# Kernel optimization log

Hardware: AMD Instinct MI355X
Metric: run time of the kernel (lower is better)

Reference implementation:

```python
import jax
import jax.numpy as jnp
from jax import lax
import numpy as np

HEADS = 12
GROUPS = 3
KSIZE = 5  # depthwise kernel for offset prediction


def bilinear_sample(img, grid):
    """img: (G,C,H,W); grid: (G,Hk,Wk,2) with (x,y) coords in [-1,1], align_corners=True.
    Returns (G,C,Hk*Wk). Coords are pre-clipped to [-1,1], so clamped indexing is exact."""
    G, C, H, W = img.shape
    gx = (grid[..., 0] + 1.0) * 0.5 * (W - 1)
    gy = (grid[..., 1] + 1.0) * 0.5 * (H - 1)
    x0 = jnp.floor(gx); y0 = jnp.floor(gy)
    wx1 = gx - x0; wx0 = 1.0 - wx1
    wy1 = gy - y0; wy0 = 1.0 - wy1
    x0i = jnp.clip(x0, 0, W - 1).astype(jnp.int32)
    x1i = jnp.clip(x0 + 1, 0, W - 1).astype(jnp.int32)
    y0i = jnp.clip(y0, 0, H - 1).astype(jnp.int32)
    y1i = jnp.clip(y0 + 1, 0, H - 1).astype(jnp.int32)
    flat = img.reshape(G, C, H * W)
    def gather(yi, xi):
        idx = (yi * W + xi).reshape(G, 1, -1)  # (G,1,Hk*Wk)
        return jnp.take_along_axis(flat, jnp.broadcast_to(idx, (G, C, idx.shape[-1])), axis=2)
    n = gx.shape[1] * gx.shape[2]
    w00 = (wy0 * wx0).reshape(G, 1, n); w01 = (wy0 * wx1).reshape(G, 1, n)
    w10 = (wy1 * wx0).reshape(G, 1, n); w11 = (wy1 * wx1).reshape(G, 1, n)
    return (gather(y0i, x0i) * w00 + gather(y0i, x1i) * w01 +
            gather(y1i, x0i) * w10 + gather(y1i, x1i) * w11)


def setup_inputs() -> dict:
    key = jax.random.key(0)
    ks = jax.random.split(key, 16)
    B, C, H, W = 8, 384, 32, 32
    Cg = C // GROUPS
    s = 0.02
    inp = {
        "x1": jax.random.normal(ks[0], (B, C, H, W), jnp.float32),
        "x2": jax.random.normal(ks[1], (B, C, H, W), jnp.float32),
        "wq": jax.random.normal(ks[2], (C, C), jnp.float32) * s,
        "bq": jnp.zeros((C,), jnp.float32),
        "w_off_dw": jax.random.normal(ks[3], (Cg, 1, KSIZE, KSIZE), jnp.float32) * s,
        "b_off_dw": jnp.zeros((Cg,), jnp.float32),
        "w_off_pw": jax.random.normal(ks[4], (2, Cg), jnp.float32) * s,
        "b_off_pw": jnp.zeros((2,), jnp.float32),
        "wk": jax.random.normal(ks[5], (C, C), jnp.float32) * s,
        "bk": jnp.zeros((C,), jnp.float32),
        "wv": jax.random.normal(ks[6], (C, C), jnp.float32) * s,
        "bv": jnp.zeros((C,), jnp.float32),
        "wo": jax.random.normal(ks[7], (C, C), jnp.float32) * s,
        "bo": jnp.zeros((C,), jnp.float32),
    }
    return inp


def deformable_cross_attn(x1, x2, wq, bq, w_off_dw, b_off_dw, w_off_pw, b_off_pw,
                          wk, bk, wv, bv, wo, bo):
    B, C, H, W = x1.shape
    Cg = C // GROUPS
    hc = C // HEADS
    scale = hc ** -0.5
    N = H * W
    # query projection (1x1 conv)
    q = jnp.einsum('oc,bchw->bohw', wq, x1) + bq[None, :, None, None]
    # grouped offset prediction: depthwise conv -> GELU -> 1x1 conv to 2 channels
    qg = q.reshape(B * GROUPS, Cg, H, W)
    off = lax.conv_general_dilated(qg, w_off_dw, (1, 1), 'SAME',
                                   feature_group_count=Cg,
                                   dimension_numbers=('NCHW', 'OIHW', 'NCHW'))
    off = jax.nn.gelu(off + b_off_dw[None, :, None, None])
    off = jnp.einsum('oc,bchw->bohw', w_off_pw, off) + b_off_pw[None, :, None, None]  # (B*G,2,H,W)
    dx = jnp.tanh(off[:, 0]) * (2.0 / W)
    dy = jnp.tanh(off[:, 1]) * (2.0 / H)
    ref_x = (jnp.arange(W, dtype=jnp.float32) + 0.5) / W * 2.0 - 1.0
    ref_y = (jnp.arange(H, dtype=jnp.float32) + 0.5) / H * 2.0 - 1.0
    px = jnp.clip(ref_x[None, None, :] + dx, -1.0, 1.0)
    py = jnp.clip(ref_y[None, :, None] + dy, -1.0, 1.0)
    grid = jnp.stack([px, py], axis=-1)  # (B*G,H,W,2)
    # sample key/value source at deformed positions
    x2g = x2.reshape(B * GROUPS, Cg, H, W)
    sampled = bilinear_sample(x2g, grid).reshape(B, C, N)
    k = jnp.einsum('oc,bcn->bon', wk, sampled) + bk[None, :, None]
    v = jnp.einsum('oc,bcn->bon', wv, sampled) + bv[None, :, None]
    qf = q.reshape(B, HEADS, hc, N)
    kf = k.reshape(B, HEADS, hc, N)
    vf = v.reshape(B, HEADS, hc, N)
    attn = jax.nn.softmax(jnp.einsum('bhcn,bhcm->bhnm', qf, kf) * scale, axis=-1)
    out = jnp.einsum('bhnm,bhcm->bhcn', attn, vf).reshape(B, C, H, W)
    y = jnp.einsum('oc,bchw->bohw', wo, out) + bo[None, :, None, None]
    return x1 + y, attn


def reference(x1, x2, wq, bq, w_off_dw, b_off_dw, w_off_pw, b_off_pw,
              wk, bk, wv, bv, wo, bo):
    return deformable_cross_attn(x1, x2, wq, bq, w_off_dw, b_off_dw,
                                 w_off_pw, b_off_pw, wk, bk, wv, bv, wo, bo)
```

## Files before the change

kernel.cpp:

```cpp
#include <hip/hip_runtime.h>
#include <hip/hip_bf16.h>

static constexpr int B = 8;
static constexpr int C = 384;
static constexpr int H = 32;
static constexpr int W = 32;
static constexpr int N = 1024;
static constexpr int Cg = 128;
static constexpr int HEADS = 12;
static constexpr int BG = 24;
static constexpr float SCALE = 0.17677669529663687f;

typedef short bf16x8 __attribute__((ext_vector_type(8)));
typedef float f32x4 __attribute__((ext_vector_type(4)));

__device__ __forceinline__ unsigned short bf16_bits(float x) {
    __hip_bfloat16 h = __float2bfloat16(x);
    return __builtin_bit_cast(unsigned short, h);
}
__device__ __forceinline__ float bf2f(unsigned short u) {
    return __builtin_bit_cast(float, ((unsigned)u) << 16);
}
__device__ __forceinline__ float fast_tanh(float x) {
    float e = __expf(2.0f * x);
    return 1.0f - 2.0f / (e + 1.0f);
}

__global__ __launch_bounds__(256) void prep(const float* __restrict__ wq,
                                            const float* __restrict__ wk,
                                            const float* __restrict__ wv,
                                            const float* __restrict__ wo,
                                            const float* __restrict__ x1,
                                            unsigned short* __restrict__ w16,
                                            unsigned short* __restrict__ x1T)
{
    __shared__ float tile[32][132];
    const int bx = blockIdx.x;
    const int tid = threadIdx.x;
    if (bx < 288) {
        int which = bx / 72, blk = bx - which*72;
        const float* src = (which == 0) ? wq : (which == 1) ? wk : (which == 2) ? wv : wo;
        int idx = (blk*256 + tid) * 8;
        const float4* p = (const float4*)(src + idx);
        float4 f0 = p[0], f1 = p[1];
        uint4 u;
        u.x = (unsigned)bf16_bits(f0.x) | ((unsigned)bf16_bits(f0.y) << 16);
        u.y = (unsigned)bf16_bits(f0.z) | ((unsigned)bf16_bits(f0.w) << 16);
        u.z = (unsigned)bf16_bits(f1.x) | ((unsigned)bf16_bits(f1.y) << 16);
        u.w = (unsigned)bf16_bits(f1.z) | ((unsigned)bf16_bits(f1.w) << 16);
        *(uint4*)(w16 + (size_t)which * 147456 + idx) = u;
        return;
    }
    const int xi = bx - 288;
    const int n0 = (xi & 7) * 128;
    const int t = xi >> 3;
    const int c0 = (t % 12) * 32;
    const int b = t / 12;
    {
        int c = tid >> 3, nq = (tid & 7) * 16;
        const float* sp = x1 + ((size_t)b*C + c0 + c)*N + n0 + nq;
        #pragma unroll
        for (int i = 0; i < 4; ++i)
            *(float4*)&tile[c][nq + 4*i] = *(const float4*)(sp + 4*i);
    }
    __syncthreads();
    {
        int n = tid >> 1, cb = (tid & 1) * 16;
        unsigned short* dp = x1T + ((size_t)b*N + n0 + n)*C + c0 + cb;
        #pragma unroll
        for (int half = 0; half < 2; ++half) {
            bf16x8 v;
            #pragma unroll
            for (int j = 0; j < 8; ++j)
                v[j] = (short)bf16_bits(tile[cb + half*8 + j][n]);
            *(bf16x8*)(dp + half*8) = v;
        }
    }
}

template<int MODE>
__global__ __launch_bounds__(256) void proj_mfma(const unsigned short* __restrict__ XT,
                                                 const unsigned short* __restrict__ Wb,
                                                 const float* __restrict__ bias,
                                                 const float* __restrict__ res,
                                                 void* __restrict__ out,
                                                 void* __restrict__ out2)
{
    __shared__ __align__(16) char smem[64*72*2*2];
    unsigned short* sA = (unsigned short*)smem;
    unsigned short* sB = sA + 64*72;
    float* ep = (float*)smem;

    const int tid = threadIdx.x;
    const int lane = tid & 63, w = tid >> 6;
    const int l15 = lane & 15, lq = lane >> 4;
    const int n0 = blockIdx.x * 64, o0 = blockIdx.y * 64, b = blockIdx.z;
    const int qn = (w & 1) * 32, qo = (w >> 1) * 32;

    const unsigned short* xg = XT + ((size_t)b*N + n0)*C;
    const unsigned short* wg = Wb + (size_t)o0*C;

    const f32x4 zero = {0.f, 0.f, 0.f, 0.f};
    f32x4 a00 = zero, a01 = zero, a10 = zero, a11 = zero;

    const int r = tid >> 2, c8 = (tid & 3) * 8;
    for (int c0 = 0; c0 < C; c0 += 64) {
        __syncthreads();
        *(bf16x8*)(sA + r*72 + c8)      = *(const bf16x8*)(xg + (size_t)r*C + c0 + c8);
        *(bf16x8*)(sA + r*72 + c8 + 32) = *(const bf16x8*)(xg + (size_t)r*C + c0 + c8 + 32);
        *(bf16x8*)(sB + r*72 + c8)      = *(const bf16x8*)(wg + (size_t)r*C + c0 + c8);
        *(bf16x8*)(sB + r*72 + c8 + 32) = *(const bf16x8*)(wg + (size_t)r*C + c0 + c8 + 32);
        __syncthreads();
        #pragma unroll
        for (int ks = 0; ks < 2; ++ks) {
            bf16x8 fa0 = *(const bf16x8*)(sA + (qn + l15)*72      + ks*32 + lq*8);
            bf16x8 fa1 = *(const bf16x8*)(sA + (qn + 16 + l15)*72 + ks*32 + lq*8);
            bf16x8 fb0 = *(const bf16x8*)(sB + (qo + l15)*72      + ks*32 + lq*8);
            bf16x8 fb1 = *(const bf16x8*)(sB + (qo + 16 + l15)*72 + ks*32 + lq*8);
            a00 = __builtin_amdgcn_mfma_f32_16x16x32_bf16(fa0, fb0, a00, 0, 0, 0);
            a01 = __builtin_amdgcn_mfma_f32_16x16x32_bf16(fa0, fb1, a01, 0, 0, 0);
            a10 = __builtin_amdgcn_mfma_f32_16x16x32_bf16(fa1, fb0, a10, 0, 0, 0);
            a11 = __builtin_amdgcn_mfma_f32_16x16x32_bf16(fa1, fb1, a11, 0, 0, 0);
        }
    }
    __syncthreads();
    #pragma unroll
    for (int rr = 0; rr < 4; ++rr) {
        int nr0 = qn + 4*lq + rr, nr1 = qn + 16 + 4*lq + rr;
        ep[nr0*65 + qo + l15]      = a00[rr];
        ep[nr0*65 + qo + 16 + l15] = a01[rr];
        ep[nr1*65 + qo + l15]      = a10[rr];
        ep[nr1*65 + qo + 16 + l15] = a11[rr];
    }
    __syncthreads();

    if constexpr (MODE == 3) {
        {
            int n = tid >> 2, ch = tid & 3;
            unsigned short* op = (unsigned short*)out + ((size_t)b*N + n0 + n)*C + o0;
            #pragma unroll
            for (int half = 0; half < 2; ++half) {
                int ob = ch*8 + half*32;
                bf16x8 v;
                #pragma unroll
                for (int j = 0; j < 8; ++j)
                    v[j] = (short)bf16_bits(ep[n*65 + ob + j] + bias[o0 + ob + j]);
                *(bf16x8*)(op + ob) = v;
            }
        }
        {
            int o = tid >> 2, nc = (tid & 3) * 16;
            float bz = bias[o0 + o];
            unsigned short* dp = (unsigned short*)out2 + ((size_t)b*C + o0 + o)*N + n0 + nc;
            #pragma unroll
            for (int half = 0; half < 2; ++half) {
                bf16x8 v;
                #pragma unroll
                for (int j = 0; j < 8; ++j)
                    v[j] = (short)bf16_bits(ep[(nc + half*8 + j)*65 + o] + bz);
                *(bf16x8*)(dp + half*8) = v;
            }
        }
    } else {
        int o = tid >> 2, nc = (tid & 3) * 16;
        float bz = bias[o0 + o];
        size_t base = ((size_t)b*C + o0 + o)*N + n0 + nc;
        #pragma unroll
        for (int i = 0; i < 4; ++i) {
            float4 rv = *(const float4*)(res + base + 4*i);
            f32x4 v;
            v[0] = ep[(nc + 4*i + 0)*65 + o] + bz + rv.x;
            v[1] = ep[(nc + 4*i + 1)*65 + o] + bz + rv.y;
            v[2] = ep[(nc + 4*i + 2)*65 + o] + bz + rv.z;
            v[3] = ep[(nc + 4*i + 3)*65 + o] + bz + rv.w;
            __builtin_nontemporal_store(v, (f32x4*)((float*)out + base + 4*i));
        }
    }
}

__global__ __launch_bounds__(256) void proj_kv(const unsigned short* __restrict__ XT,
                                               const unsigned short* __restrict__ Wk,
                                               const float* __restrict__ bk,
                                               const unsigned short* __restrict__ Wv,
                                               const float* __restrict__ bv,
                                               unsigned short* __restrict__ K16,
                                               unsigned short* __restrict__ V16)
{
    __shared__ __align__(16) char smem[64*72*2*3];
    unsigned short* sA  = (unsigned short*)smem;
    unsigned short* sBk = sA + 64*72;
    unsigned short* sBv = sA + 2*64*72;
    float* ep = (float*)smem;

    const int tid = threadIdx.x;
    const int lane = tid & 63, w = tid >> 6;
    const int l15 = lane & 15, lq = lane >> 4;
    const int n0 = blockIdx.x * 64, o0 = blockIdx.y * 64, b = blockIdx.z;
    const int qn = (w & 1) * 32, qo = (w >> 1) * 32;

    const unsigned short* xg = XT + ((size_t)b*N + n0)*C;
    const unsigned short* wkg = Wk + (size_t)o0*C;
    const unsigned short* wvg = Wv + (size_t)o0*C;

    const f32x4 zero = {0.f, 0.f, 0.f, 0.f};
    f32x4 k00 = zero, k01 = zero, k10 = zero, k11 = zero;
    f32x4 v00 = zero, v01 = zero, v10 = zero, v11 = zero;

    const int r = tid >> 2, c8 = (tid & 3) * 8;
    for (int c0 = 0; c0 < C; c0 += 64) {
        __syncthreads();
        *(bf16x8*)(sA  + r*72 + c8)      = *(const bf16x8*)(xg  + (size_t)r*C + c0 + c8);
        *(bf16x8*)(sA  + r*72 + c8 + 32) = *(const bf16x8*)(xg  + (size_t)r*C + c0 + c8 + 32);
        *(bf16x8*)(sBk + r*72 + c8)      = *(const bf16x8*)(wkg + (size_t)r*C + c0 + c8);
        *(bf16x8*)(sBk + r*72 + c8 + 32) = *(const bf16x8*)(wkg + (size_t)r*C + c0 + c8 + 32);
        *(bf16x8*)(sBv + r*72 + c8)      = *(const bf16x8*)(wvg + (size_t)r*C + c0 + c8);
        *(bf16x8*)(sBv + r*72 + c8 + 32) = *(const bf16x8*)(wvg + (size_t)r*C + c0 + c8 + 32);
        __syncthreads();
        #pragma unroll
        for (int ks = 0; ks < 2; ++ks) {
            bf16x8 fa0 = *(const bf16x8*)(sA + (qn + l15)*72      + ks*32 + lq*8);
            bf16x8 fa1 = *(const bf16x8*)(sA + (qn + 16 + l15)*72 + ks*32 + lq*8);
            bf16x8 fk0 = *(const bf16x8*)(sBk + (qo + l15)*72      + ks*32 + lq*8);
            bf16x8 fk1 = *(const bf16x8*)(sBk + (qo + 16 + l15)*72 + ks*32 + lq*8);
            bf16x8 fv0 = *(const bf16x8*)(sBv + (qo + l15)*72      + ks*32 + lq*8);
            bf16x8 fv1 = *(const bf16x8*)(sBv + (qo + 16 + l15)*72 + ks*32 + lq*8);
            k00 = __builtin_amdgcn_mfma_f32_16x16x32_bf16(fa0, fk0, k00, 0, 0, 0);
            k01 = __builtin_amdgcn_mfma_f32_16x16x32_bf16(fa0, fk1, k01, 0, 0, 0);
            k10 = __builtin_amdgcn_mfma_f32_16x16x32_bf16(fa1, fk0, k10, 0, 0, 0);
            k11 = __builtin_amdgcn_mfma_f32_16x16x32_bf16(fa1, fk1, k11, 0, 0, 0);
            v00 = __builtin_amdgcn_mfma_f32_16x16x32_bf16(fa0, fv0, v00, 0, 0, 0);
            v01 = __builtin_amdgcn_mfma_f32_16x16x32_bf16(fa0, fv1, v01, 0, 0, 0);
            v10 = __builtin_amdgcn_mfma_f32_16x16x32_bf16(fa1, fv0, v10, 0, 0, 0);
            v11 = __builtin_amdgcn_mfma_f32_16x16x32_bf16(fa1, fv1, v11, 0, 0, 0);
        }
    }
    __syncthreads();
    #pragma unroll
    for (int rr = 0; rr < 4; ++rr) {
        int nr0 = qn + 4*lq + rr, nr1 = qn + 16 + 4*lq + rr;
        ep[nr0*65 + qo + l15]      = k00[rr];
        ep[nr0*65 + qo + 16 + l15] = k01[rr];
        ep[nr1*65 + qo + l15]      = k10[rr];
        ep[nr1*65 + qo + 16 + l15] = k11[rr];
    }
    __syncthreads();
    {
        int n = tid >> 2, ch = tid & 3;
        unsigned short* op = K16 + ((size_t)b*N + n0 + n)*C + o0;
        #pragma unroll
        for (int half = 0; half < 2; ++half) {
            int ob = ch*8 + half*32;
            bf16x8 v;
            #pragma unroll
            for (int j = 0; j < 8; ++j)
                v[j] = (short)bf16_bits((ep[n*65 + ob + j] + bk[o0 + ob + j]) * SCALE);
            *(bf16x8*)(op + ob) = v;
        }
    }
    __syncthreads();
    #pragma unroll
    for (int rr = 0; rr < 4; ++rr) {
        int nr0 = qn + 4*lq + rr, nr1 = qn + 16 + 4*lq + rr;
        ep[nr0*65 + qo + l15]      = v00[rr];
        ep[nr0*65 + qo + 16 + l15] = v01[rr];
        ep[nr1*65 + qo + l15]      = v10[rr];
        ep[nr1*65 + qo + 16 + l15] = v11[rr];
    }
    __syncthreads();
    {
        int o = tid >> 2, nc = (tid & 3) * 16;
        float bz = bv[o0 + o];
        unsigned short* op = V16 + ((size_t)b*C + o0 + o)*N + n0 + nc;
        #pragma unroll
        for (int half = 0; half < 2; ++half) {
            bf16x8 v;
            #pragma unroll
            for (int j = 0; j < 8; ++j)
                v[j] = (short)bf16_bits(ep[(nc + half*8 + j)*65 + o] + bz);
            *(bf16x8*)(op + half*8) = v;
        }
    }
}

__global__ __launch_bounds__(256) void dwconv_gelu(const unsigned short* __restrict__ q,
                                                   const float* __restrict__ wdw,
                                                   const float* __restrict__ bdw,
                                                   unsigned short* __restrict__ t)
{
    __shared__ float tile[12][32];
    __shared__ float wsm[25];
    const int bx = blockIdx.x;
    const int c = blockIdx.y, bg = blockIdx.z;
    const int tid = threadIdx.x;
    const unsigned short* qc = q + ((size_t)bg*Cg + c)*N;
    if (tid < 384) {
        int row = tid >> 5, col = tid & 31;
        int gy = bx*8 - 2 + row;
        tile[row][col] = (gy >= 0 && gy < H) ? bf2f(qc[gy*W + col]) : 0.0f;
    }
    if (tid < 25) wsm[tid] = wdw[c*25 + tid];
    __syncthreads();
    const int yl = tid >> 5, x = tid & 31;
    float acc = bdw[c];
    #pragma unroll
    for (int ky = 0; ky < 5; ++ky) {
        #pragma unroll
        for (int kx = 0; kx < 5; ++kx) {
            int xx = x + kx - 2;
            if (xx < 0 || xx >= W) continue;
            acc += wsm[ky*5 + kx] * tile[yl + ky][xx];
        }
    }
    float u = acc;
    float g = 0.5f*u*(1.0f + fast_tanh(0.7978845608028654f*(u + 0.044715f*u*u*u)));
    t[((size_t)bg*Cg + c)*N + bx*256 + tid] = bf16_bits(g);
}

__global__ __launch_bounds__(256) void offbilin(const unsigned short* __restrict__ t,
                                                const float* __restrict__ wpw,
                                                const float* __restrict__ bpw,
                                                const float* __restrict__ x2,
                                                unsigned short* __restrict__ sampT)
{
    __shared__ float r0[4][64], r1[4][64];
    __shared__ float4 cbuf[64];
    __shared__ unsigned short st[64][130];
    const int tid = threadIdx.x;
    const int n0 = blockIdx.x * 64, bg = blockIdx.y;
    const int nl = tid & 63, cq = tid >> 6;
    {
        const unsigned short* tb = t + ((size_t)bg*Cg + cq*32)*N + n0 + nl;
        float a0 = 0.f, a1 = 0.f;
        #pragma unroll 8
        for (int i = 0; i < 32; ++i) {
            float tv = bf2f(tb[(size_t)i*N]);
            a0 += wpw[cq*32 + i] * tv;
            a1 += wpw[Cg + cq*32 + i] * tv;
        }
        r0[cq][nl] = a0; r1[cq][nl] = a1;
    }
    __syncthreads();
    if (tid < 64) {
        int n = n0 + nl;
        const int x = n & 31, y = n >> 5;
        float a0 = bpw[0] + r0[0][nl] + r0[1][nl] + r0[2][nl] + r0[3][nl];
        float a1 = bpw[1] + r1[0][nl] + r1[1][nl] + r1[2][nl] + r1[3][nl];
        float dx = fast_tanh(a0) * (2.0f / W);
        float dy = fast_tanh(a1) * (2.0f / H);
        float rx = (x + 0.5f) / W * 2.0f - 1.0f;
        float ry = (y + 0.5f) / H * 2.0f - 1.0f;
        float px = fminf(fmaxf(rx + dx, -1.0f), 1.0f);
        float py = fminf(fmaxf(ry + dy, -1.0f), 1.0f);
        float gx = (px + 1.0f) * 0.5f * (W - 1);
        float gy = (py + 1.0f) * 0.5f * (H - 1);
        float x0 = floorf(gx), y0 = floorf(gy);
        float wx1 = gx - x0, wy1 = gy - y0;
        x0 = fminf(fmaxf(x0, 0.0f), (float)(W - 1));
        y0 = fminf(fmaxf(y0, 0.0f), (float)(H - 1));
        cbuf[nl] = make_float4(x0, y0, wx1, wy1);
    }
    __syncthreads();
    {
        float4 c4 = cbuf[nl];
        int x0 = (int)c4.x, y0 = (int)c4.y;
        float wx1 = c4.z, wy1 = c4.w;
        int x1 = min(x0 + 1, W - 1), y1 = min(y0 + 1, H - 1);
        float wx0 = 1.0f - wx1, wy0 = 1.0f - wy1;
        const float* base = x2 + (size_t)bg*Cg*N;
        #pragma unroll 4
        for (int i = 0; i < 32; ++i) {
            int c = cq*32 + i;
            const float* img = base + (size_t)c*N;
            float v00 = img[y0*W + x0], v01 = img[y0*W + x1];
            float v10 = img[y1*W + x0], v11 = img[y1*W + x1];
            float v = wy0*(wx0*v00 + wx1*v01) + wy1*(wx0*v10 + wx1*v11);
            st[nl][c] = bf16_bits(v);
        }
    }
    __syncthreads();
    {
        int b = bg / 3, g = bg % 3;
        int nn = tid >> 2;
        unsigned short* dp = sampT + ((size_t)b*N + n0 + nn)*C + g*Cg;
        #pragma unroll
        for (int i = 0; i < 4; ++i) {
            int c8 = ((tid & 3) + 4*i) * 8;
            *(bf16x8*)(dp + c8) = *(const bf16x8*)&st[nn][c8];
        }
    }
}

__global__ __launch_bounds__(256) void attn_fused(const unsigned short* __restrict__ Q16,
                                                  const unsigned short* __restrict__ K16,
                                                  const unsigned short* __restrict__ V16,
                                                  float* __restrict__ attn,
                                                  unsigned short* __restrict__ OT)
{
    __shared__ __align__(16) unsigned short ks[256*40];
    __shared__ __align__(16) unsigned short vs[32*264];
    __shared__ __align__(16) unsigned short ps[4][16*72];

    const int tid = threadIdx.x;
    const int lane = tid & 63, w = tid >> 6;
    const int l15 = lane & 15, lq = lane >> 4;
    const int id = blockIdx.x;
    const int xcd = id & 7, j = id >> 3;
    const int bh = xcd*12 + (j >> 4);
    const int nb = j & 15;
    const int b = bh / HEADS, h = bh - b*HEADS;

    const unsigned short* qg = Q16 + ((size_t)b*N + nb*64)*C + h*32;
    const unsigned short* kg = K16 + (size_t)b*N*C + h*32;
    const unsigned short* vg = V16 + ((size_t)b*C + h*32)*N;

    const bf16x8 qfrag = *(const bf16x8*)(qg + (size_t)(w*16 + l15)*C + lq*8);

    const f32x4 zero = {0.f, 0.f, 0.f, 0.f};
    float sm = 0.f;
    f32x4 s[16];

    for (int ch = 0; ch < 4; ++ch) {
        __syncthreads();
        #pragma unroll
        for (int i = 0; i < 4; ++i) {
            int m = i*64 + (tid >> 2), c8 = (tid & 3) * 8;
            *(bf16x8*)(ks + m*40 + c8) = *(const bf16x8*)(kg + ((size_t)ch*256 + m)*C + c8);
        }
        __syncthreads();
        #pragma unroll
        for (int t = 0; t < 16; ++t) {
            bf16x8 kfrag = *(const bf16x8*)(ks + (16*t + l15)*40 + lq*8);
            s[t] = __builtin_amdgcn_mfma_f32_16x16x32_bf16(kfrag, qfrag, zero, 0, 0, 0);
        }
        float es = 0.f;
        #pragma unroll
        for (int t = 0; t < 16; ++t) {
            es += __expf(s[t][0]); es += __expf(s[t][1]);
            es += __expf(s[t][2]); es += __expf(s[t][3]);
        }
        sm += es;
    }
    sm += __shfl_xor(sm, 16);
    sm += __shfl_xor(sm, 32);
    const float inv = 1.0f / sm;

    f32x4 outf[2] = {zero, zero};
    unsigned short* pw = ps[w];
    float* abase = attn + ((size_t)bh*N + (size_t)nb*64 + w*16)*N;
    const int trow = lane >> 4;
    const int tcol = (lane & 15) * 4;

    for (int ch = 0; ch < 4; ++ch) {
        __syncthreads();
        #pragma unroll
        for (int i = 0; i < 4; ++i) {
            int m = i*64 + (tid >> 2), c8 = (tid & 3) * 8;
            *(bf16x8*)(ks + m*40 + c8) = *(const bf16x8*)(kg + ((size_t)ch*256 + m)*C + c8);
        }
        #pragma unroll
        for (int i = 0; i < 4; ++i) {
            int u = tid + i*256;
            int cl = u >> 5, gg = u & 31;
            *(bf16x8*)(vs + cl*264 + gg*8) = *(const bf16x8*)(vg + (size_t)cl*N + ch*256 + gg*8);
        }
        __syncthreads();
        #pragma unroll
        for (int t = 0; t < 16; ++t) {
            bf16x8 kfrag = *(const bf16x8*)(ks + (16*t + l15)*40 + lq*8);
            s[t] = __builtin_amdgcn_mfma_f32_16x16x32_bf16(kfrag, qfrag, zero, 0, 0, 0);
        }
        #pragma unroll
        for (int qr = 0; qr < 4; ++qr) {
            #pragma unroll
            for (int tt = 0; tt < 4; ++tt) {
                int t = qr*4 + tt;
                float e0 = __expf(s[t][0]), e1 = __expf(s[t][1]);
                float e2 = __expf(s[t][2]), e3 = __expf(s[t][3]);
                uint2 pb;
                pb.x = (unsigned)bf16_bits(e0) | ((unsigned)bf16_bits(e1) << 16);
                pb.y = (unsigned)bf16_bits(e2) | ((unsigned)bf16_bits(e3) << 16);
                *(uint2*)(pw + l15*72 + 16*tt + 4*lq) = pb;
            }
            __asm volatile("" ::: "memory");
            #pragma unroll
            for (int kk = 0; kk < 2; ++kk) {
                bf16x8 pa = *(const bf16x8*)(pw + l15*72 + kk*32 + lq*8);
                #pragma unroll
                for (int ct = 0; ct < 2; ++ct) {
                    bf16x8 vb = *(const bf16x8*)(vs + (16*ct + l15)*264 + qr*64 + kk*32 + lq*8);
                    outf[ct] = __builtin_amdgcn_mfma_f32_16x16x32_bf16(pa, vb, outf[ct], 0, 0, 0);
                }
            }
            #pragma unroll
            for (int it = 0; it < 4; ++it) {
                int row = it*4 + trow;
                uint2 u = *(const uint2*)(pw + row*72 + tcol);
                float invr = __shfl(inv, row);
                f32x4 p;
                p[0] = __builtin_bit_cast(float, u.x << 16) * invr;
                p[1] = __builtin_bit_cast(float, u.x & 0xffff0000u) * invr;
                p[2] = __builtin_bit_cast(float, u.y << 16) * invr;
                p[3] = __builtin_bit_cast(float, u.y & 0xffff0000u) * invr;
                __builtin_nontemporal_store(p,
                    (f32x4*)(abase + (size_t)row*N + ch*256 + qr*64 + tcol));
            }
            __asm volatile("" ::: "memory");
        }
    }

    float* sc = (float*)pw;
    #pragma unroll
    for (int r = 0; r < 4; ++r) {
        float invr = __shfl(inv, 4*lq + r);
        sc[(4*lq + r)*33 + l15]      = outf[0][r] * invr;
        sc[(4*lq + r)*33 + 16 + l15] = outf[1][r] * invr;
    }
    __asm volatile("" ::: "memory");
    {
        int n = lane >> 2, c8 = (lane & 3) * 8;
        bf16x8 v;
        #pragma unroll
        for (int j2 = 0; j2 < 8; ++j2)
            v[j2] = (short)bf16_bits(sc[n*33 + c8 + j2]);
        *(bf16x8*)(OT + ((size_t)b*N + nb*64 + w*16 + n)*C + h*32 + c8) = v;
    }
}

extern "C" void kernel_launch(void* const* d_in, const int* in_sizes, int n_in,
                              void* d_out, int out_size, void* d_ws, size_t ws_size,
                              hipStream_t stream)
{
    const float* x1  = (const float*)d_in[0];
    const float* x2  = (const float*)d_in[1];
    const float* wq  = (const float*)d_in[2];
    const float* bq  = (const float*)d_in[3];
    const float* wdw = (const float*)d_in[4];
    const float* bdw = (const float*)d_in[5];
    const float* wpw = (const float*)d_in[6];
    const float* bpw = (const float*)d_in[7];
    const float* wk  = (const float*)d_in[8];
    const float* bk  = (const float*)d_in[9];
    const float* wv  = (const float*)d_in[10];
    const float* bv  = (const float*)d_in[11];
    const float* wo  = (const float*)d_in[12];
    const float* bo  = (const float*)d_in[13];

    const size_t P = (size_t)B * C * N;
    float* ws = (float*)d_ws;
    unsigned short* Q16   = (unsigned short*)ws;
    unsigned short* qspat = (unsigned short*)(ws + P/2);
    unsigned short* sampT = (unsigned short*)(ws + P);
    unsigned short* K16   = (unsigned short*)(ws + 3*P/2);
    unsigned short* V16   = (unsigned short*)(ws + 2*P);
    unsigned short* x1T   = (unsigned short*)(ws + 5*P/2);
    unsigned short* OT    = x1T;
    unsigned short* tbuf  = (unsigned short*)(ws + 3*P);
    unsigned short* w16   = (unsigned short*)(ws + 7*P/2);
    unsigned short* w16q = w16;
    unsigned short* w16k = w16 + 147456;
    unsigned short* w16v = w16 + 2*147456;
    unsigned short* w16o = w16 + 3*147456;

    float* ybuf = (float*)d_out;
    float* attn = (float*)d_out + P;

    prep<<<dim3(1056), 256, 0, stream>>>(wq, wk, wv, wo, x1, w16, x1T);
    proj_mfma<3><<<dim3(16, 6, 8), 256, 0, stream>>>(x1T, w16q, bq, nullptr, Q16, qspat);
    dwconv_gelu<<<dim3(4, Cg, BG), 256, 0, stream>>>(qspat, wdw, bdw, tbuf);
    offbilin<<<dim3(16, BG), 256, 0, stream>>>(tbuf, wpw, bpw, x2, sampT);
    proj_kv<<<dim3(16, 6, 8), 256, 0, stream>>>(sampT, w16k, bk, w16v, bv, K16, V16);
    attn_fused<<<dim3(1536), 256, 0, stream>>>(Q16, K16, V16, attn, OT);
    proj_mfma<2><<<dim3(16, 6, 8), 256, 0, stream>>>(OT, w16o, bo, x1, ybuf, nullptr);
}
```

Before: 156.2 us.

## Load K/V fragments directly from global memory and use exp2 with prescaled keys

```diff
diff --git a/kernel.cpp b/kernel.cpp
--- a/kernel.cpp
+++ b/kernel.cpp
@@ -10,6 +10,7 @@
 static constexpr int HEADS = 12;
 static constexpr int BG = 24;
 static constexpr float SCALE = 0.17677669529663687f;
+static constexpr float LOG2E = 1.4426950408889634f;
 
 typedef short bf16x8 __attribute__((ext_vector_type(8)));
 typedef float f32x4 __attribute__((ext_vector_type(4)));
@@ -253,7 +254,7 @@
             bf16x8 v;
             #pragma unroll
             for (int j = 0; j < 8; ++j)
-                v[j] = (short)bf16_bits((ep[n*65 + ob + j] + bk[o0 + ob + j]) * SCALE);
+                v[j] = (short)bf16_bits((ep[n*65 + ob + j] + bk[o0 + ob + j]) * (SCALE * LOG2E));
             *(bf16x8*)(op + ob) = v;
         }
     }
@@ -396,8 +397,6 @@
                                                   float* __restrict__ attn,
                                                   unsigned short* __restrict__ OT)
 {
-    __shared__ __align__(16) unsigned short ks[256*40];
-    __shared__ __align__(16) unsigned short vs[32*264];
     __shared__ __align__(16) unsigned short ps[4][16*72];
 
     const int tid = threadIdx.x;
@@ -420,23 +419,16 @@
     f32x4 s[16];
 
     for (int ch = 0; ch < 4; ++ch) {
-        __syncthreads();
-        #pragma unroll
-        for (int i = 0; i < 4; ++i) {
-            int m = i*64 + (tid >> 2), c8 = (tid & 3) * 8;
-            *(bf16x8*)(ks + m*40 + c8) = *(const bf16x8*)(kg + ((size_t)ch*256 + m)*C + c8);
-        }
-        __syncthreads();
         #pragma unroll
         for (int t = 0; t < 16; ++t) {
-            bf16x8 kfrag = *(const bf16x8*)(ks + (16*t + l15)*40 + lq*8);
+            bf16x8 kfrag = *(const bf16x8*)(kg + (size_t)(ch*256 + 16*t + l15)*C + lq*8);
             s[t] = __builtin_amdgcn_mfma_f32_16x16x32_bf16(kfrag, qfrag, zero, 0, 0, 0);
         }
         float es = 0.f;
         #pragma unroll
         for (int t = 0; t < 16; ++t) {
-            es += __expf(s[t][0]); es += __expf(s[t][1]);
-            es += __expf(s[t][2]); es += __expf(s[t][3]);
+            es += exp2f(s[t][0]); es += exp2f(s[t][1]);
+            es += exp2f(s[t][2]); es += exp2f(s[t][3]);
         }
         sm += es;
     }
@@ -451,22 +443,9 @@
     const int tcol = (lane & 15) * 4;
 
     for (int ch = 0; ch < 4; ++ch) {
-        __syncthreads();
-        #pragma unroll
-        for (int i = 0; i < 4; ++i) {
-            int m = i*64 + (tid >> 2), c8 = (tid & 3) * 8;
-            *(bf16x8*)(ks + m*40 + c8) = *(const bf16x8*)(kg + ((size_t)ch*256 + m)*C + c8);
-        }
-        #pragma unroll
-        for (int i = 0; i < 4; ++i) {
-            int u = tid + i*256;
-            int cl = u >> 5, gg = u & 31;
-            *(bf16x8*)(vs + cl*264 + gg*8) = *(const bf16x8*)(vg + (size_t)cl*N + ch*256 + gg*8);
-        }
-        __syncthreads();
         #pragma unroll
         for (int t = 0; t < 16; ++t) {
-            bf16x8 kfrag = *(const bf16x8*)(ks + (16*t + l15)*40 + lq*8);
+            bf16x8 kfrag = *(const bf16x8*)(kg + (size_t)(ch*256 + 16*t + l15)*C + lq*8);
             s[t] = __builtin_amdgcn_mfma_f32_16x16x32_bf16(kfrag, qfrag, zero, 0, 0, 0);
         }
         #pragma unroll
@@ -474,8 +453,8 @@
             #pragma unroll
             for (int tt = 0; tt < 4; ++tt) {
                 int t = qr*4 + tt;
-                float e0 = __expf(s[t][0]), e1 = __expf(s[t][1]);
-                float e2 = __expf(s[t][2]), e3 = __expf(s[t][3]);
+                float e0 = exp2f(s[t][0]), e1 = exp2f(s[t][1]);
+                float e2 = exp2f(s[t][2]), e3 = exp2f(s[t][3]);
                 uint2 pb;
                 pb.x = (unsigned)bf16_bits(e0) | ((unsigned)bf16_bits(e1) << 16);
                 pb.y = (unsigned)bf16_bits(e2) | ((unsigned)bf16_bits(e3) << 16);
@@ -487,7 +466,8 @@
                 bf16x8 pa = *(const bf16x8*)(pw + l15*72 + kk*32 + lq*8);
                 #pragma unroll
                 for (int ct = 0; ct < 2; ++ct) {
-                    bf16x8 vb = *(const bf16x8*)(vs + (16*ct + l15)*264 + qr*64 + kk*32 + lq*8);
+                    bf16x8 vb = *(const bf16x8*)(vg + (size_t)(16*ct + l15)*N
+                                                 + ch*256 + qr*64 + kk*32 + lq*8);
                     outf[ct] = __builtin_amdgcn_mfma_f32_16x16x32_bf16(pa, vb, outf[ct], 0, 0, 0);
                 }
             }
```

Result: slower. 226.6 us (+45.1%).
